# Kernel optimization log

Hardware: AMD Instinct MI355X
Metric: run time of the kernel (lower is better)

## Reference

```python
import jax, jax.numpy as jnp
import numpy as np

N_NODES = 100000
N_EDGES = 500000
NODE_IN = 16
HID = 128
EDGE_IN = 1
NUM_STACKED = 4  # layers 1..4 share shapes; layer 0 maps NODE_IN -> HID


def setup_inputs() -> dict:
    key = jax.random.key(0)
    ks = jax.random.split(key, 16)

    def p(k, shape, fan_in):
        return (jax.random.normal(k, shape, dtype=jnp.float32) / np.float32(np.sqrt(fan_in)))

    inp = {}
    inp["x"] = jax.random.normal(ks[0], (N_NODES, NODE_IN), dtype=jnp.float32)
    inp["edge_index"] = jax.random.randint(ks[1], (2, N_EDGES), 0, N_NODES)
    inp["edge_attr"] = jax.random.normal(ks[2], (N_EDGES, EDGE_IN), dtype=jnp.float32)
    # GINE layer 0 (NODE_IN -> HID): edge lin maps EDGE_IN -> NODE_IN (PyG GINEConv.lin)
    inp["We0"] = p(ks[3], (EDGE_IN, NODE_IN), EDGE_IN)
    inp["be0"] = jnp.zeros((NODE_IN,), jnp.float32)
    inp["W10"] = p(ks[4], (NODE_IN, HID), NODE_IN)
    inp["b10"] = jnp.zeros((HID,), jnp.float32)
    inp["W20"] = p(ks[5], (HID, HID), HID)
    inp["b20"] = jnp.zeros((HID,), jnp.float32)
    # GINE layers 1..4 (HID -> HID), stacked on leading axis
    inp["We_s"] = p(ks[6], (NUM_STACKED, EDGE_IN, HID), EDGE_IN)
    inp["be_s"] = jnp.zeros((NUM_STACKED, HID), jnp.float32)
    inp["W1_s"] = p(ks[7], (NUM_STACKED, HID, HID), HID)
    inp["b1_s"] = jnp.zeros((NUM_STACKED, HID), jnp.float32)
    inp["W2_s"] = p(ks[8], (NUM_STACKED, HID, HID), HID)
    inp["b2_s"] = jnp.zeros((NUM_STACKED, HID), jnp.float32)
    # edge predictor: Linear(2*HID, HID) -> ELU -> Linear(HID, 1)
    inp["Wp1"] = p(ks[9], (2 * HID, HID), 2 * HID)
    inp["bp1"] = jnp.zeros((HID,), jnp.float32)
    inp["Wp2"] = p(ks[10], (HID, 1), HID)
    inp["bp2"] = jnp.zeros((1,), jnp.float32)
    return inp


def _gine(x, src, dst, eattr, We, be, W1, b1, W2, b2):
    # PyG GINEConv: aggr_i = sum_{(j->i)} ReLU(x_j + lin(edge_attr)); out = nn((1+eps)*x + aggr), eps=0
    m = jax.nn.relu(x[src] + eattr @ We + be)                 # [E, d] gathered messages
    aggr = jax.ops.segment_sum(m, dst, num_segments=x.shape[0])  # scatter-add to targets
    h = x + aggr
    return jax.nn.elu(h @ W1 + b1) @ W2 + b2                  # nn = Linear-ELU-Linear


def reference(x, edge_index, edge_attr, We0, be0, W10, b10, W20, b20,
              We_s, be_s, W1_s, b1_s, W2_s, b2_s, Wp1, bp1, Wp2, bp2):
    src, dst = edge_index[0], edge_index[1]
    # dropout is identity at inference (eval mode)
    h = jax.nn.elu(_gine(x, src, dst, edge_attr, We0, be0, W10, b10, W20, b20))
    for l in range(NUM_STACKED):
        h = jax.nn.elu(_gine(h, src, dst, edge_attr,
                             We_s[l], be_s[l], W1_s[l], b1_s[l], W2_s[l], b2_s[l]))
    ef = jnp.concatenate([h[src], h[dst]], axis=1)            # [E, 2*HID]
    out = jax.nn.elu(ef @ Wp1 + bp1) @ Wp2 + bp2              # [E, 1]
    return out[:, 0]
```

## Files before the change

### kernel.cpp

```cpp
#include <hip/hip_runtime.h>

#define N_NODES 100000
#define N_EDGES 500000
#define NODE_IN 16
#define HID 128
#define LPAD 140
#define SCAN_CHUNK 1024
#define NB_SCAN ((N_NODES + SCAN_CHUNK - 1) / SCAN_CHUNK)
#define DBINS 1024

typedef __attribute__((ext_vector_type(8))) short short8;
typedef __attribute__((ext_vector_type(4))) float f32x4;

__device__ __forceinline__ float elu_f(float v) {
    return v > 0.f ? v : __expf(v) - 1.f;
}

__device__ __forceinline__ unsigned short f2b(float f) {
    unsigned int u = __float_as_uint(f);
    unsigned int r = (u + 0x7fffu + ((u >> 16) & 1u)) >> 16;
    return (unsigned short)r;
}
__device__ __forceinline__ float b2f(unsigned short h) {
    return __uint_as_float((unsigned int)h << 16);
}
__device__ __forceinline__ unsigned short f2h(float f) {
    _Float16 h = (_Float16)f;
    unsigned short u;
    __builtin_memcpy(&u, &h, 2);
    return u;
}
__device__ __forceinline__ float h2f(unsigned short u) {
    _Float16 h;
    __builtin_memcpy(&h, &u, 2);
    return (float)h;
}

__global__ void deg_count_kernel(const int* __restrict__ ei, int* __restrict__ deg) {
    int e = blockIdx.x * 256 + threadIdx.x;
    if (e < N_EDGES) atomicAdd(&deg[ei[N_EDGES + e]], 1);
}

__global__ __launch_bounds__(1024) void scanA_kernel(const int* __restrict__ deg, int* __restrict__ bsum) {
    __shared__ int s[SCAN_CHUNK];
    int i = blockIdx.x * SCAN_CHUNK + threadIdx.x;
    s[threadIdx.x] = (i < N_NODES) ? deg[i] : 0;
    __syncthreads();
    for (int off = SCAN_CHUNK / 2; off > 0; off >>= 1) {
        if (threadIdx.x < off) s[threadIdx.x] += s[threadIdx.x + off];
        __syncthreads();
    }
    if (threadIdx.x == 0) bsum[blockIdx.x] = s[0];
}

__global__ void scanB_kernel(const int* __restrict__ bsum, int* __restrict__ boff,
                             int* __restrict__ rowPtr) {
    if (threadIdx.x == 0 && blockIdx.x == 0) {
        int r = 0;
        for (int i = 0; i < NB_SCAN; i++) { boff[i] = r; r += bsum[i]; }
        rowPtr[N_NODES] = N_EDGES;
    }
}

__global__ __launch_bounds__(1024) void scanC_kernel(const int* __restrict__ deg,
                                                     const int* __restrict__ boff,
                                                     int* __restrict__ rowPtr,
                                                     int* __restrict__ cursor) {
    __shared__ int bufA[SCAN_CHUNK], bufB[SCAN_CHUNK];
    int i = blockIdx.x * SCAN_CHUNK + threadIdx.x;
    int t = threadIdx.x;
    bufA[t] = (i < N_NODES) ? deg[i] : 0;
    __syncthreads();
    int* src = bufA; int* dst = bufB;
    for (int off = 1; off < SCAN_CHUNK; off <<= 1) {
        dst[t] = (t >= off) ? (src[t - off] + src[t]) : src[t];
        __syncthreads();
        int* tmp = src; src = dst; dst = tmp;
    }
    if (i < N_NODES) {
        int excl = (t == 0) ? 0 : src[t - 1];
        int v = excl + boff[blockIdx.x];
        rowPtr[i] = v;
        cursor[i] = v;
    }
}

__global__ void fill_kernel(const int* __restrict__ ei, const float* __restrict__ ea,
                            int* __restrict__ cursor, int2* __restrict__ edgeP) {
    int e = blockIdx.x * 256 + threadIdx.x;
    if (e < N_EDGES) {
        int d = ei[N_EDGES + e];
        int p = atomicAdd(&cursor[d], 1);
        edgeP[p] = make_int2(ei[e], __float_as_int(ea[e]));
    }
}

__global__ __launch_bounds__(1024) void s1_blockhist_kernel(const int* __restrict__ deg,
                                                            int* __restrict__ blockHist) {
    __shared__ int h[DBINS];
    int t = threadIdx.x, b = blockIdx.x;
    h[t] = 0;
    __syncthreads();
    int i = b * SCAN_CHUNK + t;
    if (i < N_NODES) atomicAdd(&h[min(deg[i], DBINS - 1)], 1);
    __syncthreads();
    blockHist[b * DBINS + t] = h[t];
}

__global__ __launch_bounds__(1024) void s2_scan_kernel(int* __restrict__ blockHist) {
    __shared__ int bufA[DBINS], bufB[DBINS];
    int k = threadIdx.x;
    int r = 0;
    for (int b = 0; b < NB_SCAN; b++) {
        int v = blockHist[b * DBINS + k];
        blockHist[b * DBINS + k] = r;
        r += v;
    }
    bufA[k] = r;
    __syncthreads();
    int* src = bufA; int* dst = bufB;
    for (int off = 1; off < DBINS; off <<= 1) {
        dst[k] = (k >= off) ? (src[k - off] + src[k]) : src[k];
        __syncthreads();
        int* tmp = src; src = dst; dst = tmp;
    }
    int binStart = (k == 0) ? 0 : src[k - 1];
    for (int b = 0; b < NB_SCAN; b++)
        blockHist[b * DBINS + k] += binStart;
}

__global__ __launch_bounds__(1024) void s3_scatter_kernel(const int* __restrict__ deg,
                                                          const int* __restrict__ blockHist,
                                                          int* __restrict__ perm) {
    __shared__ int cur[DBINS];
    int t = threadIdx.x, b = blockIdx.x;
    cur[t] = blockHist[b * DBINS + t];
    __syncthreads();
    int i = b * SCAN_CHUNK + t;
    if (i < N_NODES) {
        int k = min(deg[i], DBINS - 1);
        int p = atomicAdd(&cur[k], 1);
        perm[p] = i;
    }
}

__global__ __launch_bounds__(256) void pack_w_kernel(const float* __restrict__ W, int K_off,
                                                     unsigned short* __restrict__ hi,
                                                     unsigned short* __restrict__ lo)
{
    int gid = blockIdx.x * 256 + threadIdx.x;
    if (gid >= 4 * 8 * 64) return;
    int lane = gid & 63, tl = (gid >> 6) & 7, ch = gid >> 9;
    int kb = ch * 32 + (lane >> 4) * 8;
    int n  = tl * 16 + (lane & 15);
    for (int j = 0; j < 8; j++) {
        float w = W[(size_t)(K_off + kb + j) * 128 + n];
        unsigned short h = f2b(w);
        hi[(size_t)gid * 8 + j] = h;
        lo[(size_t)gid * 8 + j] = f2b(w - b2f(h));
    }
}

__global__ __launch_bounds__(256) void scatter0_kernel(
    const float* __restrict__ x, const int* __restrict__ ei,
    const float* __restrict__ ea, const float* __restrict__ We0,
    const float* __restrict__ be0, float* __restrict__ aggr)
{
    int idx = blockIdx.x * 256 + threadIdx.x;
    int e = idx >> 4, c = idx & 15;
    int s = ei[e], d = ei[N_EDGES + e];
    float m = x[s * NODE_IN + c] + ea[e] * We0[c] + be0[c];
    m = fmaxf(m, 0.f);
    atomicAdd(&aggr[d * NODE_IN + c], m);
}

__device__ __forceinline__ void fma4x4(float (&acc)[4][4],
    const float4& r0, const float4& r1, const float4& r2, const float4& r3,
    const float4& w0, const float4& w1, const float4& w2, const float4& w3)
{
    float r[4][4] = {{r0.x, r0.y, r0.z, r0.w}, {r1.x, r1.y, r1.z, r1.w},
                     {r2.x, r2.y, r2.z, r2.w}, {r3.x, r3.y, r3.z, r3.w}};
    float w[4][4] = {{w0.x, w0.y, w0.z, w0.w}, {w1.x, w1.y, w1.z, w1.w},
                     {w2.x, w2.y, w2.z, w2.w}, {w3.x, w3.y, w3.z, w3.w}};
#pragma unroll
    for (int i = 0; i < 4; i++)
#pragma unroll
        for (int k = 0; k < 4; k++)
#pragma unroll
            for (int c = 0; c < 4; c++)
                acc[i][c] = fmaf(r[i][k], w[k][c], acc[i][c]);
}

__global__ __launch_bounds__(256) void mlp0_kernel(
    const float* __restrict__ x, const float* __restrict__ aggr,
    const float* __restrict__ W1, const float* __restrict__ b1,
    const float* __restrict__ W2, const float* __restrict__ b2,
    unsigned short* __restrict__ h)
{
    __shared__ float in0[32][20];
    __shared__ float mid[32][HID];
    const int t = threadIdx.x;
    const int q = t & 31, g = t >> 5;
    const int c0 = q * 4;
    const int base = blockIdx.x * 32;

    for (int i = t; i < 32 * NODE_IN; i += 256) {
        int r = i >> 4, cc = i & 15;
        int n = base + r;
        in0[r][cc] = x[n * NODE_IN + cc] + aggr[n * NODE_IN + cc];
    }
    __syncthreads();

    float4 bb = *(const float4*)&b1[c0];
    float acc[4][4];
#pragma unroll
    for (int i = 0; i < 4; i++) { acc[i][0] = bb.x; acc[i][1] = bb.y; acc[i][2] = bb.z; acc[i][3] = bb.w; }
    for (int k = 0; k < NODE_IN; k += 4) {
        float4 r0 = *(const float4*)&in0[g * 4 + 0][k];
        float4 r1 = *(const float4*)&in0[g * 4 + 1][k];
        float4 r2 = *(const float4*)&in0[g * 4 + 2][k];
        float4 r3 = *(const float4*)&in0[g * 4 + 3][k];
        float4 w0 = *(const float4*)&W1[(k + 0) * HID + c0];
        float4 w1 = *(const float4*)&W1[(k + 1) * HID + c0];
        float4 w2 = *(const float4*)&W1[(k + 2) * HID + c0];
        float4 w3 = *(const float4*)&W1[(k + 3) * HID + c0];
        fma4x4(acc, r0, r1, r2, r3, w0, w1, w2, w3);
    }
#pragma unroll
    for (int i = 0; i < 4; i++)
        *(float4*)&mid[g * 4 + i][c0] = make_float4(elu_f(acc[i][0]), elu_f(acc[i][1]),
                                                    elu_f(acc[i][2]), elu_f(acc[i][3]));
    __syncthreads();

    float4 bb2 = *(const float4*)&b2[c0];
    float acc2[4][4];
#pragma unroll
    for (int i = 0; i < 4; i++) { acc2[i][0] = bb2.x; acc2[i][1] = bb2.y; acc2[i][2] = bb2.z; acc2[i][3] = bb2.w; }
    for (int k = 0; k < HID; k += 4) {
        float4 r0 = *(const float4*)&mid[g * 4 + 0][k];
        float4 r1 = *(const float4*)&mid[g * 4 + 1][k];
        float4 r2 = *(const float4*)&mid[g * 4 + 2][k];
        float4 r3 = *(const float4*)&mid[g * 4 + 3][k];
        float4 w0 = *(const float4*)&W2[(k + 0) * HID + c0];
        float4 w1 = *(const float4*)&W2[(k + 1) * HID + c0];
        float4 w2 = *(const float4*)&W2[(k + 2) * HID + c0];
        float4 w3 = *(const float4*)&W2[(k + 3) * HID + c0];
        fma4x4(acc2, r0, r1, r2, r3, w0, w1, w2, w3);
    }
#pragma unroll
    for (int i = 0; i < 4; i++) {
        ushort4 o;
        o.x = f2h(elu_f(acc2[i][0])); o.y = f2h(elu_f(acc2[i][1]));
        o.z = f2h(elu_f(acc2[i][2])); o.w = f2h(elu_f(acc2[i][3]));
        *(ushort4*)&h[(size_t)(base + g * 4 + i) * HID + c0] = o;
    }
}

__device__ __forceinline__ void afrag_split(const float (&buf)[16][LPAD], int lane,
                                            short8 (&ah)[4], short8 (&al)[4])
{
    const int m = lane & 15, s8 = (lane >> 4) * 8;
#pragma unroll
    for (int ch = 0; ch < 4; ch++) {
        float4 a0 = *(const float4*)&buf[m][ch * 32 + s8];
        float4 a1 = *(const float4*)&buf[m][ch * 32 + s8 + 4];
        float av[8] = {a0.x, a0.y, a0.z, a0.w, a1.x, a1.y, a1.z, a1.w};
#pragma unroll
        for (int j = 0; j < 8; j++) {
            unsigned short h = f2b(av[j]);
            ah[ch][j] = (short)h;
            al[ch][j] = (short)f2b(av[j] - b2f(h));
        }
    }
}

template <bool PRED>
__global__ __launch_bounds__(64) void gine_mfma_kernel(
    const unsigned short* __restrict__ hin, const int* __restrict__ rowPtr,
    const int2* __restrict__ edgeP, const int* __restrict__ perm,
    const float* __restrict__ We, const float* __restrict__ be,
    const unsigned short* __restrict__ W1h, const unsigned short* __restrict__ W1l,
    const float* __restrict__ b1,
    const unsigned short* __restrict__ W2h, const unsigned short* __restrict__ W2l,
    const float* __restrict__ b2,
    unsigned short* __restrict__ hout,
    const unsigned short* __restrict__ P1h, const unsigned short* __restrict__ P1l,
    const unsigned short* __restrict__ P2h, const unsigned short* __restrict__ P2l,
    unsigned short* __restrict__ Pbuf)
{
    __shared__ float buf[16][LPAD];
    const int lane = threadIdx.x;
    const int qg = lane & 15, rg = lane >> 4;
    const int c0 = qg * 8;
    const int base = blockIdx.x * 16;

    float wev[8], bev[8];
#pragma unroll
    for (int j = 0; j < 8; j++) { wev[j] = We[c0 + j]; bev[j] = be[c0 + j]; }

    int nn[4], s0[4], e0[4];
    float acc[4][8];
#pragma unroll
    for (int i = 0; i < 4; i++) {
        nn[i] = perm[base + rg * 4 + i];
        s0[i] = rowPtr[nn[i]];
        e0[i] = rowPtr[nn[i] + 1];
        short8 h0 = *(const short8*)&hin[(size_t)nn[i] * HID + c0];
#pragma unroll
        for (int j = 0; j < 8; j++) acc[i][j] = h2f((unsigned short)h0[j]);
    }
    int maxd = 0;
#pragma unroll
    for (int i = 0; i < 4; i++) maxd = max(maxd, e0[i] - s0[i]);

    int idx[8]; float av[8]; bool act[8];
#pragma unroll
    for (int u = 0; u < 2; u++)
#pragma unroll
        for (int i = 0; i < 4; i++) {
            int slot = u * 4 + i;
            int j = s0[i] + u;
            act[slot] = j < e0[i];
            int jc = act[slot] ? j : (N_EDGES - 1);
            int2 ep = edgeP[jc];
            idx[slot] = ep.x;
            av[slot]  = __int_as_float(ep.y);
        }

    for (int sb = 0; sb < maxd; sb += 2) {
        short8 hraw[8];
#pragma unroll
        for (int s = 0; s < 8; s++)
            hraw[s] = *(const short8*)&hin[(size_t)idx[s] * HID + c0];

        int nidx[8]; float nav[8]; bool nact[8];
#pragma unroll
        for (int u = 0; u < 2; u++)
#pragma unroll
            for (int i = 0; i < 4; i++) {
                int slot = u * 4 + i;
                int j = s0[i] + sb + 2 + u;
                nact[slot] = j < e0[i];
                int jc = nact[slot] ? j : (N_EDGES - 1);
                int2 ep = edgeP[jc];
                nidx[slot] = ep.x;
                nav[slot]  = __int_as_float(ep.y);
            }

#pragma unroll
        for (int u = 0; u < 2; u++)
#pragma unroll
            for (int i = 0; i < 4; i++) {
                int slot = u * 4 + i;
                if (act[slot]) {
#pragma unroll
                    for (int j = 0; j < 8; j++) {
                        float hv = h2f((unsigned short)hraw[slot][j]);
                        acc[i][j] += fmaxf(fmaf(av[slot], wev[j], bev[j]) + hv, 0.f);
                    }
                }
            }
#pragma unroll
        for (int s = 0; s < 8; s++) {
            idx[s] = nidx[s]; av[s] = nav[s]; act[s] = nact[s];
        }
    }
#pragma unroll
    for (int i = 0; i < 4; i++) {
        *(float4*)&buf[rg * 4 + i][c0]     = make_float4(acc[i][0], acc[i][1], acc[i][2], acc[i][3]);
        *(float4*)&buf[rg * 4 + i][c0 + 4] = make_float4(acc[i][4], acc[i][5], acc[i][6], acc[i][7]);
    }
    __syncthreads();

    const int col16 = lane & 15, r0 = (lane >> 4) * 4;

    {
        short8 ah[4], al[4];
        afrag_split(buf, lane, ah, al);
        float res[8][4];
#pragma unroll
        for (int tl = 0; tl < 8; tl++) {
            int col = tl * 16 + col16;
            float bv = b1[col];
            f32x4 c = {bv, bv, bv, bv};
#pragma unroll
            for (int ch = 0; ch < 4; ch++) {
                int off = ((ch * 8 + tl) * 64 + lane) * 8;
                short8 bh = *(const short8*)&W1h[off];
                short8 bl = *(const short8*)&W1l[off];
                c = __builtin_amdgcn_mfma_f32_16x16x32_bf16(ah[ch], bh, c, 0, 0, 0);
                c = __builtin_amdgcn_mfma_f32_16x16x32_bf16(al[ch], bh, c, 0, 0, 0);
                c = __builtin_amdgcn_mfma_f32_16x16x32_bf16(ah[ch], bl, c, 0, 0, 0);
            }
#pragma unroll
            for (int r = 0; r < 4; r++) res[tl][r] = elu_f(c[r]);
        }
        __syncthreads();
#pragma unroll
        for (int tl = 0; tl < 8; tl++)
#pragma unroll
            for (int r = 0; r < 4; r++)
                buf[r0 + r][tl * 16 + col16] = res[tl][r];
    }
    __syncthreads();

    {
        short8 ah[4], al[4];
        afrag_split(buf, lane, ah, al);
        float res[8][4];
#pragma unroll
        for (int tl = 0; tl < 8; tl++) {
            int col = tl * 16 + col16;
            float bv = b2[col];
            f32x4 c = {bv, bv, bv, bv};
#pragma unroll
            for (int ch = 0; ch < 4; ch++) {
                int off = ((ch * 8 + tl) * 64 + lane) * 8;
                short8 bh = *(const short8*)&W2h[off];
                short8 bl = *(const short8*)&W2l[off];
                c = __builtin_amdgcn_mfma_f32_16x16x32_bf16(ah[ch], bh, c, 0, 0, 0);
                c = __builtin_amdgcn_mfma_f32_16x16x32_bf16(al[ch], bh, c, 0, 0, 0);
                c = __builtin_amdgcn_mfma_f32_16x16x32_bf16(ah[ch], bl, c, 0, 0, 0);
            }
#pragma unroll
            for (int r = 0; r < 4; r++) res[tl][r] = elu_f(c[r]);
        }
        __syncthreads();
#pragma unroll
        for (int tl = 0; tl < 8; tl++)
#pragma unroll
            for (int r = 0; r < 4; r++)
                buf[r0 + r][tl * 16 + col16] = res[tl][r];
    }
    __syncthreads();

    if constexpr (!PRED) {
#pragma unroll
        for (int i = 0; i < 4; i++) {
            short8 o;
#pragma unroll
            for (int j = 0; j < 8; j++) o[j] = (short)f2h(buf[rg * 4 + i][c0 + j]);
            *(short8*)&hout[(size_t)nn[i] * HID + c0] = o;
        }
    } else {
        short8 ah[4], al[4];
        afrag_split(buf, lane, ah, al);
        int pn[4];
#pragma unroll
        for (int r = 0; r < 4; r++) pn[r] = perm[base + r0 + r];
#pragma unroll
        for (int tl = 0; tl < 8; tl++) {
            int col = tl * 16 + col16;
            f32x4 c1 = {0.f, 0.f, 0.f, 0.f};
            f32x4 c2 = {0.f, 0.f, 0.f, 0.f};
#pragma unroll
            for (int ch = 0; ch < 4; ch++) {
                int off = ((ch * 8 + tl) * 64 + lane) * 8;
                short8 bh1 = *(const short8*)&P1h[off];
                short8 bl1 = *(const short8*)&P1l[off];
                c1 = __builtin_amdgcn_mfma_f32_16x16x32_bf16(ah[ch], bh1, c1, 0, 0, 0);
                c1 = __builtin_amdgcn_mfma_f32_16x16x32_bf16(al[ch], bh1, c1, 0, 0, 0);
                c1 = __builtin_amdgcn_mfma_f32_16x16x32_bf16(ah[ch], bl1, c1, 0, 0, 0);
                short8 bh2 = *(const short8*)&P2h[off];
                short8 bl2 = *(const short8*)&P2l[off];
                c2 = __builtin_amdgcn_mfma_f32_16x16x32_bf16(ah[ch], bh2, c2, 0, 0, 0);
                c2 = __builtin_amdgcn_mfma_f32_16x16x32_bf16(al[ch], bh2, c2, 0, 0, 0);
                c2 = __builtin_amdgcn_mfma_f32_16x16x32_bf16(ah[ch], bl2, c2, 0, 0, 0);
            }
#pragma unroll
            for (int r = 0; r < 4; r++) {
                size_t n = (size_t)pn[r];
                Pbuf[n * 256 + col]       = f2b(c1[r]);
                Pbuf[n * 256 + 128 + col] = f2b(c2[r]);
            }
        }
    }
}

__global__ __launch_bounds__(256) void pred_edge_kernel(
    const unsigned short* __restrict__ Pbuf, const int* __restrict__ ei,
    const float* __restrict__ bp1, const float* __restrict__ Wp2,
    const float* __restrict__ bp2, float* __restrict__ out)
{
    const int t = threadIdx.x;
    const int lane = t & 31;
    const int eloc = t >> 5;
    const int e = blockIdx.x * 8 + eloc;
    const int c0 = lane * 4;

    int s = ei[e], d = ei[N_EDGES + e];
    ushort4 ua = *(const ushort4*)&Pbuf[(size_t)s * 256 + c0];
    ushort4 ub = *(const ushort4*)&Pbuf[(size_t)d * 256 + 128 + c0];
    float4 bb = *(const float4*)&bp1[c0];
    float4 w = *(const float4*)&Wp2[c0];
    float r = elu_f(b2f(ua.x) + b2f(ub.x) + bb.x) * w.x
            + elu_f(b2f(ua.y) + b2f(ub.y) + bb.y) * w.y
            + elu_f(b2f(ua.z) + b2f(ub.z) + bb.z) * w.z
            + elu_f(b2f(ua.w) + b2f(ub.w) + bb.w) * w.w;
#pragma unroll
    for (int off = 16; off > 0; off >>= 1) r += __shfl_down(r, off, 32);
    if (lane == 0) out[e] = r + bp2[0];
}

extern "C" void kernel_launch(void* const* d_in, const int* in_sizes, int n_in,
                              void* d_out, int out_size, void* d_ws, size_t ws_size,
                              hipStream_t stream) {
    const float* x    = (const float*)d_in[0];
    const int*   ei   = (const int*)d_in[1];
    const float* ea   = (const float*)d_in[2];
    const float* We0  = (const float*)d_in[3];
    const float* be0  = (const float*)d_in[4];
    const float* W10  = (const float*)d_in[5];
    const float* b10  = (const float*)d_in[6];
    const float* W20  = (const float*)d_in[7];
    const float* b20  = (const float*)d_in[8];
    const float* We_s = (const float*)d_in[9];
    const float* be_s = (const float*)d_in[10];
    const float* W1_s = (const float*)d_in[11];
    const float* b1_s = (const float*)d_in[12];
    const float* W2_s = (const float*)d_in[13];
    const float* b2_s = (const float*)d_in[14];
    const float* Wp1  = (const float*)d_in[15];
    const float* bp1  = (const float*)d_in[16];
    const float* Wp2  = (const float*)d_in[17];
    const float* bp2  = (const float*)d_in[18];
    float* out = (float*)d_out;

    unsigned short* h16A = (unsigned short*)d_ws;
    unsigned short* h16B = h16A + (size_t)N_NODES * HID;
    unsigned short* Pbuf = h16B + (size_t)N_NODES * HID;
    float* R = (float*)(Pbuf + (size_t)N_NODES * 256);

    float* aggr0 = R;
    int* deg     = (int*)(aggr0 + (size_t)N_NODES * NODE_IN);
    int* rowPtr  = deg + N_NODES;
    int* cursor  = rowPtr + N_NODES + 1;
    int2* edgeP  = (int2*)(cursor + N_NODES);
    int* bsum    = (int*)(edgeP + N_EDGES);
    int* boff    = bsum + NB_SCAN;
    int* perm    = boff + NB_SCAN;
    int* blockHist = perm + N_NODES;

    unsigned short* wpk = (unsigned short*)(R + (size_t)6 * 1024 * 1024);
    const size_t WSLOT = 16384;

    hipMemsetAsync(deg, 0, N_NODES * sizeof(int), stream);
    deg_count_kernel<<<(N_EDGES + 255) / 256, 256, 0, stream>>>(ei, deg);
    scanA_kernel<<<NB_SCAN, SCAN_CHUNK, 0, stream>>>(deg, bsum);
    scanB_kernel<<<1, 64, 0, stream>>>(bsum, boff, rowPtr);
    scanC_kernel<<<NB_SCAN, SCAN_CHUNK, 0, stream>>>(deg, boff, rowPtr, cursor);
    fill_kernel<<<(N_EDGES + 255) / 256, 256, 0, stream>>>(ei, ea, cursor, edgeP);

    s1_blockhist_kernel<<<NB_SCAN, DBINS, 0, stream>>>(deg, blockHist);
    s2_scan_kernel<<<1, DBINS, 0, stream>>>(blockHist);
    s3_scatter_kernel<<<NB_SCAN, DBINS, 0, stream>>>(deg, blockHist, perm);

    for (int l = 0; l < 4; l++) {
        pack_w_kernel<<<8, 256, 0, stream>>>(W1_s + (size_t)l * 16384, 0,
                                             wpk + (0 + l) * WSLOT, wpk + (4 + l) * WSLOT);
        pack_w_kernel<<<8, 256, 0, stream>>>(W2_s + (size_t)l * 16384, 0,
                                             wpk + (8 + l) * WSLOT, wpk + (12 + l) * WSLOT);
    }
    pack_w_kernel<<<8, 256, 0, stream>>>(Wp1, 0,   wpk + 16 * WSLOT, wpk + 17 * WSLOT);
    pack_w_kernel<<<8, 256, 0, stream>>>(Wp1, 128, wpk + 18 * WSLOT, wpk + 19 * WSLOT);

    hipMemsetAsync(aggr0, 0, (size_t)N_NODES * NODE_IN * sizeof(float), stream);
    scatter0_kernel<<<(N_EDGES * NODE_IN) / 256, 256, 0, stream>>>(x, ei, ea, We0, be0, aggr0);
    mlp0_kernel<<<N_NODES / 32, 256, 0, stream>>>(x, aggr0, W10, b10, W20, b20, h16A);

    unsigned short* hin = h16A; unsigned short* hout_ = h16B;
    for (int l = 0; l < 3; l++) {
        gine_mfma_kernel<false><<<N_NODES / 16, 64, 0, stream>>>(
            hin, rowPtr, edgeP, perm,
            We_s + l * HID, be_s + l * HID,
            wpk + (0 + l) * WSLOT, wpk + (4 + l) * WSLOT, b1_s + l * HID,
            wpk + (8 + l) * WSLOT, wpk + (12 + l) * WSLOT, b2_s + l * HID,
            hout_, nullptr, nullptr, nullptr, nullptr, nullptr);
        unsigned short* tmp = hin; hin = hout_; hout_ = tmp;
    }

    {
        const int l = 3;
        gine_mfma_kernel<true><<<N_NODES / 16, 64, 0, stream>>>(
            hin, rowPtr, edgeP, perm,
            We_s + l * HID, be_s + l * HID,
            wpk + (0 + l) * WSLOT, wpk + (4 + l) * WSLOT, b1_s + l * HID,
            wpk + (8 + l) * WSLOT, wpk + (12 + l) * WSLOT, b2_s + l * HID,
            nullptr, wpk + 16 * WSLOT, wpk + 17 * WSLOT,
            wpk + 18 * WSLOT, wpk + 19 * WSLOT, Pbuf);
    }

    pred_edge_kernel<<<N_EDGES / 8, 256, 0, stream>>>(Pbuf, ei, bp1, Wp2, bp2, out);
}
```

Baseline: 637.8 us.

## Split bin scan into parallel kernels and pack four GINE waves per block

The single-block degree-bin scan is split into three kernels: a column scan over 4 blocks, a bin-prefix scan, and a grid-wide add of each bin's start offset. This shortens the serial tail of the node-reordering setup. The GINE MFMA kernel now runs 256-thread blocks of four independent 64-lane waves, each with its own LDS slice, instead of 64-thread blocks, to reduce block count and improve occupancy. The perm array is padded with zeros so tail waves recompute node 0. That duplicate work is redundant but writes identical values.

```diff
diff --git a/kernel.cpp b/kernel.cpp
--- a/kernel.cpp
+++ b/kernel.cpp
@@ -8,6 +8,8 @@
 #define SCAN_CHUNK 1024
 #define NB_SCAN ((N_NODES + SCAN_CHUNK - 1) / SCAN_CHUNK)
 #define DBINS 1024
+#define NBLK64 1563
+#define PERM_PAD (NBLK64 * 64)
 
 typedef __attribute__((ext_vector_type(8))) short short8;
 typedef __attribute__((ext_vector_type(4))) float f32x4;
@@ -107,16 +109,25 @@
     blockHist[b * DBINS + t] = h[t];
 }
 
-__global__ __launch_bounds__(1024) void s2_scan_kernel(int* __restrict__ blockHist) {
-    __shared__ int bufA[DBINS], bufB[DBINS];
-    int k = threadIdx.x;
+__global__ __launch_bounds__(256) void s2a_colscan_kernel(int* __restrict__ blockHist,
+                                                          int* __restrict__ binTot) {
+    int k = blockIdx.x * 256 + threadIdx.x;
+    if (k >= DBINS) return;
     int r = 0;
+#pragma unroll 7
     for (int b = 0; b < NB_SCAN; b++) {
         int v = blockHist[b * DBINS + k];
         blockHist[b * DBINS + k] = r;
         r += v;
     }
-    bufA[k] = r;
+    binTot[k] = r;
+}
+
+__global__ __launch_bounds__(1024) void s2b_binscan_kernel(const int* __restrict__ binTot,
+                                                           int* __restrict__ binStart) {
+    __shared__ int bufA[DBINS], bufB[DBINS];
+    int k = threadIdx.x;
+    bufA[k] = binTot[k];
     __syncthreads();
     int* src = bufA; int* dst = bufB;
     for (int off = 1; off < DBINS; off <<= 1) {
@@ -124,9 +135,13 @@
         __syncthreads();
         int* tmp = src; src = dst; dst = tmp;
     }
-    int binStart = (k == 0) ? 0 : src[k - 1];
-    for (int b = 0; b < NB_SCAN; b++)
-        blockHist[b * DBINS + k] += binStart;
+    binStart[k] = (k == 0) ? 0 : src[k - 1];
+}
+
+__global__ __launch_bounds__(1024) void s2c_add_kernel(int* __restrict__ blockHist,
+                                                       const int* __restrict__ binStart) {
+    int g = blockIdx.x * 1024 + threadIdx.x;
+    if (g < NB_SCAN * DBINS) blockHist[g] += binStart[g & (DBINS - 1)];
 }
 
 __global__ __launch_bounds__(1024) void s3_scatter_kernel(const int* __restrict__ deg,
@@ -275,7 +290,7 @@
 }
 
 template <bool PRED>
-__global__ __launch_bounds__(64) void gine_mfma_kernel(
+__global__ __launch_bounds__(256, 4) void gine_mfma_kernel(
     const unsigned short* __restrict__ hin, const int* __restrict__ rowPtr,
     const int2* __restrict__ edgeP, const int* __restrict__ perm,
     const float* __restrict__ We, const float* __restrict__ be,
@@ -288,11 +303,13 @@
     const unsigned short* __restrict__ P2h, const unsigned short* __restrict__ P2l,
     unsigned short* __restrict__ Pbuf)
 {
-    __shared__ float buf[16][LPAD];
-    const int lane = threadIdx.x;
+    __shared__ float bufAll[4][16][LPAD];
+    const int w = threadIdx.x >> 6;
+    const int lane = threadIdx.x & 63;
+    float (&buf)[16][LPAD] = bufAll[w];
     const int qg = lane & 15, rg = lane >> 4;
     const int c0 = qg * 8;
-    const int base = blockIdx.x * 16;
+    const int base = blockIdx.x * 64 + w * 16;
 
     float wev[8], bev[8];
 #pragma unroll
@@ -539,7 +556,9 @@
     int* bsum    = (int*)(edgeP + N_EDGES);
     int* boff    = bsum + NB_SCAN;
     int* perm    = boff + NB_SCAN;
-    int* blockHist = perm + N_NODES;
+    int* blockHist = perm + PERM_PAD;
+    int* binTot   = blockHist + NB_SCAN * DBINS;
+    int* binStart = binTot + DBINS;
 
     unsigned short* wpk = (unsigned short*)(R + (size_t)6 * 1024 * 1024);
     const size_t WSLOT = 16384;
@@ -551,8 +570,11 @@
     scanC_kernel<<<NB_SCAN, SCAN_CHUNK, 0, stream>>>(deg, boff, rowPtr, cursor);
     fill_kernel<<<(N_EDGES + 255) / 256, 256, 0, stream>>>(ei, ea, cursor, edgeP);
 
+    hipMemsetAsync(perm, 0, PERM_PAD * sizeof(int), stream);
     s1_blockhist_kernel<<<NB_SCAN, DBINS, 0, stream>>>(deg, blockHist);
-    s2_scan_kernel<<<1, DBINS, 0, stream>>>(blockHist);
+    s2a_colscan_kernel<<<4, 256, 0, stream>>>(blockHist, binTot);
+    s2b_binscan_kernel<<<1, DBINS, 0, stream>>>(binTot, binStart);
+    s2c_add_kernel<<<NB_SCAN, 1024, 0, stream>>>(blockHist, binStart);
     s3_scatter_kernel<<<NB_SCAN, DBINS, 0, stream>>>(deg, blockHist, perm);
 
     for (int l = 0; l < 4; l++) {
@@ -570,7 +592,7 @@
 
     unsigned short* hin = h16A; unsigned short* hout_ = h16B;
     for (int l = 0; l < 3; l++) {
-        gine_mfma_kernel<false><<<N_NODES / 16, 64, 0, stream>>>(
+        gine_mfma_kernel<false><<<NBLK64, 256, 0, stream>>>(
             hin, rowPtr, edgeP, perm,
             We_s + l * HID, be_s + l * HID,
             wpk + (0 + l) * WSLOT, wpk + (4 + l) * WSLOT, b1_s + l * HID,
@@ -581,7 +603,7 @@
 
     {
         const int l = 3;
-        gine_mfma_kernel<true><<<N_NODES / 16, 64, 0, stream>>>(
+        gine_mfma_kernel<true><<<NBLK64, 256, 0, stream>>>(
             hin, rowPtr, edgeP, perm,
             We_s + l * HID, be_s + l * HID,
             wpk + (0 + l) * WSLOT, wpk + (4 + l) * WSLOT, b1_s + l * HID,
```

Result: faster. 614.6 us (-3.6%).
